# Kernel optimization log

Measured on AMD Instinct MI355X. Metric: run time of the kernel, lower is better.

## Reference

```python
import jax, jax.numpy as jnp
import numpy as np
from itertools import product as iter_product

N_QUBITS = 6
DIM = 2 ** N_QUBITS            # 64
N_GEN = DIM * DIM - 1          # 4095
DEPTH = 4
N_OBS = 15

_GENS = None

def _build_generators(n):
    I = np.eye(2, dtype=np.complex64)
    X = np.array([[0, 1], [1, 0]], np.complex64)
    Y = np.array([[0, -1j], [1j, 0]], np.complex64)
    Z = np.array([[1, 0], [0, -1]], np.complex64)
    P = [I, X, Y, Z]
    gens = []
    for idx in iter_product(range(4), repeat=n):
        if all(i == 0 for i in idx):
            continue
        m = P[idx[0]]
        for k in range(1, n):
            m = np.kron(m, P[idx[k]])
        gens.append(m)
    return jnp.asarray(np.stack(gens))  # [4^n-1, 2^n, 2^n] complex64

def _gens():
    global _GENS
    if _GENS is None:
        _GENS = _build_generators(N_QUBITS)
    return _GENS

def _apply_ry(psi, q, theta, n):
    # psi: [B, 2^n] complex; RY(theta) on qubit q
    B = psi.shape[0]
    x = psi.reshape(B, 2 ** q, 2, 2 ** (n - q - 1))
    c = jnp.cos(theta / 2)
    s = jnp.sin(theta / 2)
    s0, s1 = x[:, :, 0, :], x[:, :, 1, :]
    x = jnp.stack([c * s0 - s * s1, s * s0 + c * s1], axis=2)
    return x.reshape(B, -1)

def _apply_cnot(psi, c, t, n):
    # psi: [B, 2^n]; CNOT control c, target t
    B = psi.shape[0]
    x = psi.reshape((B,) + (2,) * n)
    ax_c, ax_t = 1 + c, 1 + t
    x0 = jnp.take(x, 0, axis=ax_c)
    x1 = jnp.take(x, 1, axis=ax_c)
    ax_t2 = ax_t - (1 if ax_t > ax_c else 0)
    x1 = jnp.flip(x1, axis=ax_t2)
    x = jnp.stack([x0, x1], axis=ax_c)
    return x.reshape(B, -1)

def _make_hermitians(A, B, D):
    # create_Hermitian vectorized over the m observables.
    # h[i,j] = A[idx]+iB[idx] for j<i (row-major lower-tri), h[i-1,i-1]=D[i];
    # then H = h + h^H.
    il, jl = jnp.tril_indices(DIM, -1)  # row-major order matches count+j loop
    di = jnp.arange(DIM - 1)

    def one(a, b, d):
        h = jnp.zeros((DIM, DIM), jnp.complex64)
        h = h.at[il, jl].set(a + 1j * b)
        h = h.at[di, di].set(d[1:].astype(jnp.complex64))
        return h + h.conj().T

    return jax.vmap(one)(A, B, D)  # [m, DIM, DIM]

def setup_inputs() -> dict:
    key = jax.random.key(0)
    ks = jax.random.split(key, 8)
    batch, input_dim, hidden = 256, 1024, 2047
    n_off = DIM * (DIM - 1) // 2  # 2016
    return {
        "x": jax.random.normal(ks[0], (batch, input_dim), jnp.float32),
        "W1": 0.02 * jax.random.normal(ks[1], (input_dim, hidden), jnp.float32),
        "b1": jnp.zeros((hidden,), jnp.float32),
        "W2": 0.02 * jax.random.normal(ks[2], (hidden, N_GEN), jnp.float32),
        "b2": jnp.zeros((N_GEN,), jnp.float32),
        "var_params": 0.01 * jax.random.normal(ks[3], (DEPTH, N_QUBITS), jnp.float32),
        "A": 2.0 * jax.random.normal(ks[4], (N_OBS, n_off), jnp.float32),
        "B": 2.0 * jax.random.normal(ks[5], (N_OBS, n_off), jnp.float32),
        "D": 2.0 * jax.random.normal(ks[6], (N_OBS, DIM), jnp.float32),
    }

def reference(x, W1, b1, W2, b2, var_params, A, B, D):
    n = N_QUBITS
    # encoding projection: Linear -> SiLU -> Linear
    h = jax.nn.silu(x @ W1 + b1)
    theta = h @ W2 + b2  # [batch, 4^n - 1]
    gens = _gens()  # [n_gen, dim, dim] complex64 (constant)
    # A_mat = sum_g theta_g G_g (Hermitian), U = exp(i A_mat)
    Amat = jnp.einsum('bg,gij->bij', theta.astype(jnp.complex64), gens)
    U = jax.vmap(jax.scipy.linalg.expm)(1j * Amat)  # [batch, dim, dim]
    psi = U[:, :, 0]  # apply to |0...0>
    # hardware-efficient VQC: RY layer + CNOT ring per depth
    for d in range(DEPTH):
        for q in range(n):
            psi = _apply_ry(psi, q, var_params[d, q], n)
        for q in range(n):
            psi = _apply_cnot(psi, q, (q + 1) % n, n)
    H = _make_hermitians(A, B, D)  # [m, dim, dim]
    # expectation <psi|H_w|psi>
    exp = jnp.einsum('bi,wij,bj->bw', psi.conj(), H, psi).real
    return exp  # [batch, n_observables]
```

## Files before the change

kernel.cpp:

```cpp
#include <hip/hip_runtime.h>
#include <math.h>

typedef unsigned short ushort_t;
typedef __attribute__((ext_vector_type(8))) short bf16x8_t;
typedef __attribute__((ext_vector_type(4))) float f32x4_t;

__device__ __forceinline__ void tsplit(float v, unsigned& h, unsigned& l) {
  unsigned u = __float_as_uint(v);
  h = u >> 16;
  float lo = v - __uint_as_float(u & 0xffff0000u);
  l = __float_as_uint(lo) >> 16;
}

__device__ __forceinline__ void split8(const float* p, bf16x8_t& hi, bf16x8_t& lo) {
#pragma unroll
  for (int e = 0; e < 8; ++e) {
    unsigned h, l;
    tsplit(p[e], h, l);
    hi[e] = (short)h;
    lo[e] = (short)l;
  }
}

#define LSTR 40

__global__ __launch_bounds__(512) void gemm1_kernel(
    const float* __restrict__ x, const float* __restrict__ W1,
    const float* __restrict__ b1,
    ushort_t* __restrict__ hh, ushort_t* __restrict__ hl) {
  __shared__ __align__(16) ushort_t As[2][32 * LSTR];
  __shared__ __align__(16) ushort_t Bs[2][64 * LSTR];
  const int t = threadIdx.x;
  const int lane = t & 63;
  const int wv = t >> 6;
  const int l15 = lane & 15;
  const int quad = lane >> 4;
  const int wm = wv & 1;
  const int wn = wv >> 1;
  const int m0 = (blockIdx.x >> 5) * 32;
  const int n0 = (blockIdx.x & 31) * 64;

  f32x4_t acc = (f32x4_t){0.f, 0.f, 0.f, 0.f};

  const int xrow = (t & 127) >> 2;
  const int xkq  = (t & 3) * 8;
  const int wu   = t - 128;
  const int wnx  = wu & 63;
  const int wkh  = (wu >> 6) & 3;
  const bool wok = (n0 + wnx) < 2047;

  for (int k0 = 0; k0 < 1024; k0 += 32) {
    if (t < 128) {
      const float* src = x + (size_t)(m0 + xrow) * 1024 + k0 + xkq;
      float p[8];
      float4 va = *(const float4*)src;
      float4 vb = *(const float4*)(src + 4);
      p[0] = va.x; p[1] = va.y; p[2] = va.z; p[3] = va.w;
      p[4] = vb.x; p[5] = vb.y; p[6] = vb.z; p[7] = vb.w;
      bf16x8_t hi, lo;
      split8(p, hi, lo);
      *(bf16x8_t*)&As[0][xrow * LSTR + xkq] = hi;
      *(bf16x8_t*)&As[1][xrow * LSTR + xkq] = lo;
    } else if (t < 384) {
      float p[8];
#pragma unroll
      for (int i = 0; i < 8; ++i) {
        int k = k0 + wkh * 8 + i;
        p[i] = wok ? W1[(size_t)k * 2047 + n0 + wnx] : 0.f;
      }
      bf16x8_t hi, lo;
      split8(p, hi, lo);
      *(bf16x8_t*)&Bs[0][wnx * LSTR + wkh * 8] = hi;
      *(bf16x8_t*)&Bs[1][wnx * LSTR + wkh * 8] = lo;
    }
    __syncthreads();
    const int nr = wn * 16 + l15;
    bf16x8_t bfh = *(const bf16x8_t*)&Bs[0][nr * LSTR + quad * 8];
    bf16x8_t bfl = *(const bf16x8_t*)&Bs[1][nr * LSTR + quad * 8];
    const int mr = wm * 16 + l15;
    bf16x8_t afh = *(const bf16x8_t*)&As[0][mr * LSTR + quad * 8];
    bf16x8_t afl = *(const bf16x8_t*)&As[1][mr * LSTR + quad * 8];
    acc = __builtin_amdgcn_mfma_f32_16x16x32_bf16(afh, bfh, acc, 0, 0, 0);
    acc = __builtin_amdgcn_mfma_f32_16x16x32_bf16(afh, bfl, acc, 0, 0, 0);
    acc = __builtin_amdgcn_mfma_f32_16x16x32_bf16(afl, bfh, acc, 0, 0, 0);
    __syncthreads();
  }
  const int col = n0 + wn * 16 + l15;
#pragma unroll
  for (int rg = 0; rg < 4; ++rg) {
    int row = m0 + wm * 16 + quad * 4 + rg;
    float v = acc[rg];
    if (col < 2047) {
      v += b1[col];
      v = v / (1.f + expf(-v));
    } else {
      v = 0.f;
    }
    unsigned h, l;
    tsplit(v, h, l);
    size_t o = (size_t)row * 2048 + col;
    hh[o] = (ushort_t)h;
    hl[o] = (ushort_t)l;
  }
}

__global__ __launch_bounds__(256) void gemm2k_kernel(
    const ushort_t* __restrict__ Ah, const ushort_t* __restrict__ Al,
    const float* __restrict__ W2,
    float* __restrict__ part) {
  __shared__ __align__(16) ushort_t Ab[2][64 * LSTR];
  __shared__ __align__(16) ushort_t Bb[2][64 * LSTR];
  const int t = threadIdx.x;
  const int lane = t & 63;
  const int wv = t >> 6;
  const int l15 = lane & 15;
  const int quad = lane >> 4;
  const int wm = wv >> 1, wn = wv & 1;
  const int m0 = blockIdx.y * 64;
  const int n0 = blockIdx.x * 64;
  const int ks = blockIdx.z;

  const int wu  = t - 128;
  const int bn  = wu & 63;
  const int bkh = (wu >> 6) & 1;
  const bool bok = (n0 + bn) < 4095;

  f32x4_t acc[2][2];
#pragma unroll
  for (int i = 0; i < 2; ++i)
#pragma unroll
    for (int j = 0; j < 2; ++j) acc[i][j] = (f32x4_t){0.f, 0.f, 0.f, 0.f};

  for (int kt = 0; kt < 16; ++kt) {
    const int k0 = ks * 512 + kt * 32;
    if (wv < 2) {
      const ushort_t* src = wv ? Al : Ah;
      ushort_t* dst = Ab[wv];
#pragma unroll
      for (int q = 0; q < 4; ++q) {
        int r = q * 16 + (lane >> 2);
        int c = (lane & 3) * 8;
        *(int4*)&dst[r * LSTR + c] =
            *(const int4*)(src + (size_t)(m0 + r) * 2048 + k0 + c);
      }
    } else {
      float p[16];
#pragma unroll
      for (int i = 0; i < 16; ++i) {
        int k = k0 + bkh * 16 + i;
        p[i] = (bok && k < 2047) ? W2[(size_t)k * 4095 + n0 + bn] : 0.f;
      }
#pragma unroll
      for (int half = 0; half < 2; ++half) {
        bf16x8_t hi, lo;
        split8(&p[half * 8], hi, lo);
        *(bf16x8_t*)&Bb[0][bn * LSTR + bkh * 16 + half * 8] = hi;
        *(bf16x8_t*)&Bb[1][bn * LSTR + bkh * 16 + half * 8] = lo;
      }
    }
    __syncthreads();
    bf16x8_t bfh[2], bfl[2];
#pragma unroll
    for (int j = 0; j < 2; ++j) {
      int nr = wn * 32 + j * 16 + l15;
      bfh[j] = *(const bf16x8_t*)&Bb[0][nr * LSTR + quad * 8];
      bfl[j] = *(const bf16x8_t*)&Bb[1][nr * LSTR + quad * 8];
    }
#pragma unroll
    for (int i = 0; i < 2; ++i) {
      int mr = wm * 32 + i * 16 + l15;
      bf16x8_t afh = *(const bf16x8_t*)&Ab[0][mr * LSTR + quad * 8];
      bf16x8_t afl = *(const bf16x8_t*)&Ab[1][mr * LSTR + quad * 8];
#pragma unroll
      for (int j = 0; j < 2; ++j) {
        acc[i][j] = __builtin_amdgcn_mfma_f32_16x16x32_bf16(
            afh, bfh[j], acc[i][j], 0, 0, 0);
        acc[i][j] = __builtin_amdgcn_mfma_f32_16x16x32_bf16(
            afh, bfl[j], acc[i][j], 0, 0, 0);
        acc[i][j] = __builtin_amdgcn_mfma_f32_16x16x32_bf16(
            afl, bfh[j], acc[i][j], 0, 0, 0);
      }
    }
    __syncthreads();
  }
  float* pbase = part + (size_t)ks * 256 * 4096;
#pragma unroll
  for (int i = 0; i < 2; ++i)
#pragma unroll
    for (int j = 0; j < 2; ++j) {
      int row0 = m0 + wm * 32 + i * 16 + quad * 4;
      int col = n0 + wn * 32 + j * 16 + l15;
#pragma unroll
      for (int rg = 0; rg < 4; ++rg)
        pbase[(size_t)(row0 + rg) * 4096 + col] = acc[i][j][rg];
    }
}

#define TM 64
#define TN 64
#define TK 16
__global__ __launch_bounds__(256) void gemm_tiled(
    const float* __restrict__ X, const float* __restrict__ W,
    const float* __restrict__ bias, float* __restrict__ out,
    int M, int N, int K, int ldx, int ldw, int ldo, int doSilu, int padN)
{
  __shared__ float Xs[TK][TM + 4];
  __shared__ float Ws[TK][TN + 4];
  const int t = threadIdx.x;
  const int n0 = blockIdx.x * TN;
  const int m0 = blockIdx.y * TM;
  const int tr = t >> 4, tc = t & 15;
  float acc[4][4];
#pragma unroll
  for (int i = 0; i < 4; ++i)
#pragma unroll
    for (int j = 0; j < 4; ++j) acc[i][j] = 0.f;
  const int xr = t >> 2, xk = (t & 3) * 4;
  const int wk = t >> 4, wc = (t & 15) * 4;
  for (int k0 = 0; k0 < K; k0 += TK) {
    {
      const float* xp = X + (size_t)(m0 + xr) * ldx + (k0 + xk);
      float xv[4];
      if (k0 + xk + 3 < K) {
        float4 v = *(const float4*)xp;
        xv[0] = v.x; xv[1] = v.y; xv[2] = v.z; xv[3] = v.w;
      } else {
#pragma unroll
        for (int e = 0; e < 4; ++e) xv[e] = (k0 + xk + e < K) ? xp[e] : 0.f;
      }
#pragma unroll
      for (int e = 0; e < 4; ++e) Xs[xk + e][xr] = xv[e];
    }
    {
      const int kk = k0 + wk;
      const float* wp = W + (size_t)kk * ldw + (n0 + wc);
      const bool kv = kk < K;
#pragma unroll
      for (int e = 0; e < 4; ++e) {
        int n = n0 + wc + e;
        Ws[wk][wc + e] = (kv && n < N) ? wp[e] : 0.f;
      }
    }
    __syncthreads();
#pragma unroll
    for (int k = 0; k < TK; ++k) {
      float4 av = *(const float4*)&Xs[k][tr * 4];
      float4 bv = *(const float4*)&Ws[k][tc * 4];
      float a4[4] = {av.x, av.y, av.z, av.w};
      float b4[4] = {bv.x, bv.y, bv.z, bv.w};
#pragma unroll
      for (int i = 0; i < 4; ++i)
#pragma unroll
        for (int j = 0; j < 4; ++j)
          acc[i][j] = fmaf(a4[i], b4[j], acc[i][j]);
    }
    __syncthreads();
  }
#pragma unroll
  for (int i = 0; i < 4; ++i) {
    const int mrow = m0 + tr * 4 + i;
    float* op = out + (size_t)mrow * ldo;
#pragma unroll
    for (int j = 0; j < 4; ++j) {
      const int n = n0 + tc * 4 + j;
      if (n < N) {
        float v = acc[i][j] + bias[n];
        if (doSilu) v = v / (1.f + expf(-v));
        op[n] = v;
      } else if (n < padN) {
        op[n] = 0.f;
      }
    }
  }
}

#define RS 72
#define PL (64 * RS)

__device__ __forceinline__ void qmm4(
    const ushort_t* __restrict__ Prm, const ushort_t* __restrict__ Qcm,
    float* ore, float* oim, int mt, int nt, int quad, int l15)
{
  f32x4_t aR = (f32x4_t){0.f, 0.f, 0.f, 0.f};
  f32x4_t aN = (f32x4_t){0.f, 0.f, 0.f, 0.f};
  f32x4_t aI = (f32x4_t){0.f, 0.f, 0.f, 0.f};
#pragma unroll
  for (int kb = 0; kb < 2; ++kb) {
    const int ko = kb * 32 + quad * 8;
    const int ra = (mt * 16 + l15) * RS + ko;
    bf16x8_t arh = *(const bf16x8_t*)&Prm[0 * PL + ra];
    bf16x8_t arl = *(const bf16x8_t*)&Prm[1 * PL + ra];
    bf16x8_t aih = *(const bf16x8_t*)&Prm[2 * PL + ra];
    bf16x8_t ail = *(const bf16x8_t*)&Prm[3 * PL + ra];
    const int rb = (nt * 16 + l15) * RS + ko;
    bf16x8_t brh = *(const bf16x8_t*)&Qcm[0 * PL + rb];
    bf16x8_t brl = *(const bf16x8_t*)&Qcm[1 * PL + rb];
    bf16x8_t bih = *(const bf16x8_t*)&Qcm[2 * PL + rb];
    bf16x8_t bil = *(const bf16x8_t*)&Qcm[3 * PL + rb];
    aR = __builtin_amdgcn_mfma_f32_16x16x32_bf16(arh, brh, aR, 0, 0, 0);
    aR = __builtin_amdgcn_mfma_f32_16x16x32_bf16(arh, brl, aR, 0, 0, 0);
    aR = __builtin_amdgcn_mfma_f32_16x16x32_bf16(arl, brh, aR, 0, 0, 0);
    aN = __builtin_amdgcn_mfma_f32_16x16x32_bf16(aih, bih, aN, 0, 0, 0);
    aN = __builtin_amdgcn_mfma_f32_16x16x32_bf16(aih, bil, aN, 0, 0, 0);
    aN = __builtin_amdgcn_mfma_f32_16x16x32_bf16(ail, bih, aN, 0, 0, 0);
    aI = __builtin_amdgcn_mfma_f32_16x16x32_bf16(arh, bih, aI, 0, 0, 0);
    aI = __builtin_amdgcn_mfma_f32_16x16x32_bf16(arh, bil, aI, 0, 0, 0);
    aI = __builtin_amdgcn_mfma_f32_16x16x32_bf16(arl, bih, aI, 0, 0, 0);
    aI = __builtin_amdgcn_mfma_f32_16x16x32_bf16(aih, brh, aI, 0, 0, 0);
    aI = __builtin_amdgcn_mfma_f32_16x16x32_bf16(aih, brl, aI, 0, 0, 0);
    aI = __builtin_amdgcn_mfma_f32_16x16x32_bf16(ail, brh, aI, 0, 0, 0);
  }
#pragma unroll
  for (int rg = 0; rg < 4; ++rg) {
    ore[rg] = aR[rg] - aN[rg];
    oim[rg] = aI[rg];
  }
}

__device__ __forceinline__ void stage_rm4(
    ushort_t* rm, const float* re, const float* im, int mt, int nt,
    int quad, int l15)
{
  unsigned rh[4], rl[4], ih[4], il[4];
#pragma unroll
  for (int rg = 0; rg < 4; ++rg) {
    tsplit(re[rg], rh[rg], rl[rg]);
    tsplit(im[rg], ih[rg], il[rg]);
  }
#pragma unroll
  for (int rg = 0; rg < 4; ++rg) {
    int idx = (mt * 16 + quad * 4 + rg) * RS + nt * 16 + l15;
    rm[0 * PL + idx] = (ushort_t)rh[rg];
    rm[1 * PL + idx] = (ushort_t)rl[rg];
    rm[2 * PL + idx] = (ushort_t)ih[rg];
    rm[3 * PL + idx] = (ushort_t)il[rg];
  }
}

__device__ __forceinline__ void stage_cm4(
    ushort_t* cm, const float* re, const float* im, int mt, int nt,
    int quad, int l15)
{
  unsigned rh[4], rl[4], ih[4], il[4];
#pragma unroll
  for (int rg = 0; rg < 4; ++rg) {
    tsplit(re[rg], rh[rg], rl[rg]);
    tsplit(im[rg], ih[rg], il[rg]);
  }
  int base = (nt * 16 + l15) * RS + mt * 16 + quad * 4;
  uint2 p;
  p.x = rh[0] | (rh[1] << 16); p.y = rh[2] | (rh[3] << 16);
  *(uint2*)&cm[0 * PL + base] = p;
  p.x = rl[0] | (rl[1] << 16); p.y = rl[2] | (rl[3] << 16);
  *(uint2*)&cm[1 * PL + base] = p;
  p.x = ih[0] | (ih[1] << 16); p.y = ih[2] | (ih[3] << 16);
  *(uint2*)&cm[2 * PL + base] = p;
  p.x = il[0] | (il[1] << 16); p.y = il[2] | (il[3] << 16);
  *(uint2*)&cm[3 * PL + base] = p;
}

__device__ __forceinline__ void stage_both4(
    ushort_t* rm, ushort_t* cm, const float* re, const float* im,
    int mt, int nt, int quad, int l15)
{
  stage_rm4(rm, re, im, mt, nt, quad, l15);
  stage_cm4(cm, re, im, mt, nt, quad, l15);
}

__global__ __launch_bounds__(1024, 4) void quantum_kernel(
    const float* __restrict__ pin,
    const float* __restrict__ b2g,
    const float* __restrict__ vp,
    const float* __restrict__ Aobs,
    const float* __restrict__ Bobs,
    const float* __restrict__ Dobs,
    float* __restrict__ out,
    int fused)
{
  __shared__ __align__(16) ushort_t PQ[2][8 * PL];
  __shared__ float ps[128];
  __shared__ float scr16[16];
  __shared__ float csb[24], snb[24];
  __shared__ float sAf;
  __shared__ int   sS;

  float*  thetas = (float*)&PQ[1][0];
  float2* Als    = (float2*)&PQ[0][0];

  const int t = threadIdx.x;
  const int b = blockIdx.x;
  const int lane = t & 63;
  const int w = t >> 6;
  const int quad = lane >> 4;
  const int l15 = lane & 15;
  const int mt = w >> 2, nt = w & 3;

  float ssq;
  {
    float4 v = ((const float4*)(pin + (size_t)b * 4096))[t];
    if (fused) {
#pragma unroll
      for (int k = 1; k < 4; ++k) {
        float4 u =
            ((const float4*)(pin + (size_t)k * 256 * 4096 + (size_t)b * 4096))[t];
        v.x += u.x; v.y += u.y; v.z += u.z; v.w += u.w;
      }
      int n0i = 4 * t;
      v.x += b2g[n0i];
      v.y += b2g[n0i + 1];
      v.z += b2g[n0i + 2];
      if (n0i + 3 < 4095) v.w += b2g[n0i + 3];
    }
    if (t == 1023) v.w = 0.f;
    thetas[4 * t + 0] = v.x; thetas[4 * t + 1] = v.y;
    thetas[4 * t + 2] = v.z; thetas[4 * t + 3] = v.w;
    ssq = v.x * v.x + v.y * v.y + v.z * v.z + v.w * v.w;
  }
#pragma unroll
  for (int mm = 1; mm < 64; mm <<= 1) ssq += __shfl_xor(ssq, mm);
  if (lane == 0) scr16[w] = ssq;
  __syncthreads();
  if (w == 0) {
    float s = (lane < 16) ? scr16[lane] : 0.f;
#pragma unroll
    for (int mm = 1; mm < 64; mm <<= 1) s += __shfl_xor(s, mm);
    if (lane == 0) {
      float frob = fmaxf(8.f * sqrtf(s), 1e-3f);
      sAf = frob;
      float bound = 0.30f * frob;
      int sc = (bound > 1.f) ? (int)ceilf(log2f(bound)) : 0;
      sS = sc < 0 ? 0 : (sc > 12 ? 12 : sc);
    }
  } else if (w == 1 && lane < 24) {
    float sn, cs;
    sincosf(vp[lane] * 0.5f, &sn, &cs);
    snb[lane] = sn;
    csb[lane] = cs;
  }
  __syncthreads();
  const int sPow = sS;

  for (int xx = 0; xx < 4; ++xx) {
    const int x = w + 16 * xx;
    const int z = lane;
    int g1 = 0;
#pragma unroll
    for (int bq = 0; bq < 6; ++bq) {
      int xb = (x >> bq) & 1, zb = (z >> bq) & 1;
      int dig = xb ? (zb ? 2 : 1) : (zb ? 3 : 0);
      g1 |= dig << (2 * bq);
    }
    float tv = (g1 == 0) ? 0.f : thetas[g1 - 1];
    int pc = __popc(x & z) & 3;
    float re, im;
    switch (pc) {
      case 0:  re = tv;  im = 0.f;  break;
      case 1:  re = 0.f; im = -tv;  break;
      case 2:  re = -tv; im = 0.f;  break;
      default: re = 0.f; im = tv;   break;
    }
#pragma unroll
    for (int mk = 1; mk < 64; mk <<= 1) {
      float ore = __shfl_xor(re, mk);
      float oim = __shfl_xor(im, mk);
      if (z & mk) { re = ore - re; im = oim - im; }
      else        { re = re + ore; im = im + oim; }
    }
    Als[z * 66 + (z ^ x)] = make_float2(re, im);
  }
  __syncthreads();

  const float scl = ldexpf(1.f, -sPow);
  float bre[4], bim[4];
#pragma unroll
  for (int rg = 0; rg < 4; ++rg) {
    int row = mt * 16 + quad * 4 + rg;
    int col = nt * 16 + l15;
    float2 v = Als[row * 66 + col];
    bre[rg] = -v.y * scl;
    bim[rg] =  v.x * scl;
  }
  __syncthreads();

  ushort_t* b0 = &PQ[0][0];
  ushort_t* b1 = &PQ[1][0];
  stage_both4(b0, b0 + 4 * PL, bre, bim, mt, nt, quad, l15);
  __syncthreads();
  float b2re[4], b2im[4];
  qmm4(b0, b0 + 4 * PL, b2re, b2im, mt, nt, quad, l15);
  stage_both4(b1, b1 + 4 * PL, b2re, b2im, mt, nt, quad, l15);
  __syncthreads();
  float b3re[4], b3im[4];
  qmm4(b1, b0 + 4 * PL, b3re, b3im, mt, nt, quad, l15);

  const float c3 = 1.f / 6.f, c4 = 1.f / 24.f, c5 = 1.f / 120.f;
  const float c6 = 1.f / 720.f, c7 = 1.f / 5040.f, c8 = 1.f / 40320.f;
  float s1re[4], s1im[4], p0re[4], p0im[4];
#pragma unroll
  for (int rg = 0; rg < 4; ++rg) {
    float dg = (mt == nt && l15 == quad * 4 + rg) ? 1.f : 0.f;
    s1re[rg] = c4 * dg + c5 * bre[rg] + c6 * b2re[rg] + c7 * b3re[rg];
    s1im[rg] =           c5 * bim[rg] + c6 * b2im[rg] + c7 * b3im[rg];
    p0re[rg] = dg + bre[rg] + 0.5f * b2re[rg] + c3 * b3re[rg];
    p0im[rg] =      bim[rg] + 0.5f * b2im[rg] + c3 * b3im[rg];
  }
  float b4re[4], b4im[4];
  qmm4(b1, b1 + 4 * PL, b4re, b4im, mt, nt, quad, l15);
#pragma unroll
  for (int rg = 0; rg < 4; ++rg) {
    s1re[rg] += c8 * b4re[rg];
    s1im[rg] += c8 * b4im[rg];
  }
  __syncthreads();
  stage_rm4(b0, s1re, s1im, mt, nt, quad, l15);
  stage_cm4(b0 + 4 * PL, b4re, b4im, mt, nt, quad, l15);
  __syncthreads();
  float ure[4], uim[4];
  qmm4(b0, b0 + 4 * PL, ure, uim, mt, nt, quad, l15);
#pragma unroll
  for (int rg = 0; rg < 4; ++rg) {
    ure[rg] += p0re[rg];
    uim[rg] += p0im[rg];
  }

  int cur = 1;
  for (int q = 0; q < sPow; ++q) {
    ushort_t* bb = &PQ[cur][0];
    stage_both4(bb, bb + 4 * PL, ure, uim, mt, nt, quad, l15);
    __syncthreads();
    qmm4(bb, bb + 4 * PL, ure, uim, mt, nt, quad, l15);
    cur ^= 1;
  }

  if (nt == 0 && l15 == 0) {
#pragma unroll
    for (int rg = 0; rg < 4; ++rg) {
      int row = mt * 16 + quad * 4 + rg;
      ps[2 * row] = ure[rg];
      ps[2 * row + 1] = uim[rg];
    }
  }
  __syncthreads();

  if (t < 64) {
    float pre = ps[2 * t], pim = ps[2 * t + 1];
#pragma unroll
    for (int d = 0; d < 4; ++d) {
#pragma unroll
      for (int q = 0; q < 6; ++q) {
        float s = snb[d * 6 + q], c = csb[d * 6 + q];
        int bpos = 5 - q;
        int bit = (t >> bpos) & 1;
        float ore = __shfl_xor(pre, 1 << bpos);
        float oim = __shfl_xor(pim, 1 << bpos);
        float sg = bit ? s : -s;
        pre = c * pre + sg * ore;
        pim = c * pim + sg * oim;
      }
#pragma unroll
      for (int q = 0; q < 6; ++q) {
        int bc = 5 - q;
        int bt = 5 - ((q + 1) % 6);
        float ore = __shfl_xor(pre, 1 << bt);
        float oim = __shfl_xor(pim, 1 << bt);
        int ctrl = (t >> bc) & 1;
        pre = ctrl ? ore : pre;
        pim = ctrl ? oim : pim;
      }
    }
    ps[2 * t] = pre; ps[2 * t + 1] = pim;
  }
  __syncthreads();

  float* Rt = (float*)&PQ[0][0];
  float* It = Rt + 2016;
  for (int p = t; p < 2016; p += 1024) {
    int i = (int)((1.f + sqrtf(8.f * (float)p + 1.f)) * 0.5f);
    while (i * (i - 1) / 2 > p) --i;
    while (i * (i + 1) / 2 <= p) ++i;
    int j = p - i * (i - 1) / 2;
    float pri = ps[2 * i], pii = ps[2 * i + 1];
    float prj = ps[2 * j], pij = ps[2 * j + 1];
    Rt[p] = pri * prj + pii * pij;
    It[p] = pri * pij - pii * prj;
  }
  __syncthreads();

  if (w < 15) {
    float xr = ps[2 * lane], xi = ps[2 * lane + 1];
    float mypsq = xr * xr + xi * xi;
    const float* Ap = Aobs + w * 2016;
    const float* Bp = Bobs + w * 2016;
    float part = 0.f;
    for (int p2 = lane; p2 < 1008; p2 += 64) {
      float2 a = *(const float2*)&Ap[2 * p2];
      float2 bb2 = *(const float2*)&Bp[2 * p2];
      float2 rt = *(const float2*)&Rt[2 * p2];
      float2 it = *(const float2*)&It[2 * p2];
      part += a.x * rt.x - bb2.x * it.x;
      part += a.y * rt.y - bb2.y * it.y;
    }
    if (lane < 63) part += Dobs[w * 64 + lane + 1] * mypsq;
#pragma unroll
    for (int mm = 1; mm < 64; mm <<= 1) part += __shfl_xor(part, mm);
    if (lane == 0) out[b * 15 + w] = 2.f * part;
  }
}

extern "C" void kernel_launch(void* const* d_in, const int* in_sizes, int n_in,
                              void* d_out, int out_size, void* d_ws, size_t ws_size,
                              hipStream_t stream) {
  const float* x  = (const float*)d_in[0];
  const float* W1 = (const float*)d_in[1];
  const float* b1 = (const float*)d_in[2];
  const float* W2 = (const float*)d_in[3];
  const float* b2 = (const float*)d_in[4];
  const float* vp = (const float*)d_in[5];
  const float* Ao = (const float*)d_in[6];
  const float* Bo = (const float*)d_in[7];
  const float* Do = (const float*)d_in[8];
  float* out = (float*)d_out;

  const size_t O_PT = 0;
  const size_t O_HH = 16777216;
  const size_t O_HL = 17825792;
  const size_t NEED = 18874368;

  if (ws_size >= NEED) {
    char* ws = (char*)d_ws;
    float* part16 = (float*)(ws + O_PT);
    ushort_t* hh  = (ushort_t*)(ws + O_HH);
    ushort_t* hl  = (ushort_t*)(ws + O_HL);

    gemm1_kernel<<<256, 512, 0, stream>>>(x, W1, b1, hh, hl);
    gemm2k_kernel<<<dim3(64, 4, 4), 256, 0, stream>>>(hh, hl, W2, part16);
    quantum_kernel<<<256, 1024, 0, stream>>>(part16, b2, vp, Ao, Bo, Do, out, 1);
  } else {
    float* h     = (float*)d_ws;
    float* theta = h + 256 * 2048;
    gemm_tiled<<<dim3(32, 4), 256, 0, stream>>>(
        x, W1, b1, h, 256, 2047, 1024, 1024, 2047, 2048, 1, 2048);
    gemm_tiled<<<dim3(64, 4), 256, 0, stream>>>(
        h, W2, b2, theta, 256, 4095, 2047, 2048, 4095, 4096, 0, 4096);
    quantum_kernel<<<256, 1024, 0, stream>>>(theta, b2, vp, Ao, Bo, Do, out, 0);
  }
}
```

Measured before the change: 174.2 us.

## Double-buffer shared tiles and prefetch next K-slice into registers in gemm2k

```diff
diff --git a/kernel.cpp b/kernel.cpp
--- a/kernel.cpp
+++ b/kernel.cpp
@@ -108,8 +108,8 @@
     const ushort_t* __restrict__ Ah, const ushort_t* __restrict__ Al,
     const float* __restrict__ W2,
     float* __restrict__ part) {
-  __shared__ __align__(16) ushort_t Ab[2][64 * LSTR];
-  __shared__ __align__(16) ushort_t Bb[2][64 * LSTR];
+  __shared__ __align__(16) ushort_t Ab[2][2][64 * LSTR];
+  __shared__ __align__(16) ushort_t Bb[2][2][64 * LSTR];
   const int t = threadIdx.x;
   const int lane = t & 63;
   const int wv = t >> 6;
@@ -124,6 +124,8 @@
   const int bn  = wu & 63;
   const int bkh = (wu >> 6) & 1;
   const bool bok = (n0 + bn) < 4095;
+  const int ar  = lane >> 2;
+  const int ac  = (lane & 3) * 8;
 
   f32x4_t acc[2][2];
 #pragma unroll
@@ -131,46 +133,69 @@
 #pragma unroll
     for (int j = 0; j < 2; ++j) acc[i][j] = (f32x4_t){0.f, 0.f, 0.f, 0.f};
 
-  for (int kt = 0; kt < 16; ++kt) {
-    const int k0 = ks * 512 + kt * 32;
+  int4  pa[4];
+  float pw[16];
+
+  {
+    const int k0 = ks * 512;
     if (wv < 2) {
       const ushort_t* src = wv ? Al : Ah;
-      ushort_t* dst = Ab[wv];
-#pragma unroll
-      for (int q = 0; q < 4; ++q) {
-        int r = q * 16 + (lane >> 2);
-        int c = (lane & 3) * 8;
-        *(int4*)&dst[r * LSTR + c] =
-            *(const int4*)(src + (size_t)(m0 + r) * 2048 + k0 + c);
-      }
+#pragma unroll
+      for (int q = 0; q < 4; ++q)
+        pa[q] = *(const int4*)(src + (size_t)(m0 + q * 16 + ar) * 2048 + k0 + ac);
     } else {
-      float p[16];
 #pragma unroll
       for (int i = 0; i < 16; ++i) {
         int k = k0 + bkh * 16 + i;
-        p[i] = (bok && k < 2047) ? W2[(size_t)k * 4095 + n0 + bn] : 0.f;
-      }
+        pw[i] = (bok && k < 2047) ? W2[(size_t)k * 4095 + n0 + bn] : 0.f;
+      }
+    }
+  }
+
+  int cur = 0;
+  for (int kt = 0; kt < 16; ++kt) {
+    if (wv < 2) {
+      ushort_t* dst = Ab[cur][wv];
+#pragma unroll
+      for (int q = 0; q < 4; ++q)
+        *(int4*)&dst[(q * 16 + ar) * LSTR + ac] = pa[q];
+    } else {
 #pragma unroll
       for (int half = 0; half < 2; ++half) {
         bf16x8_t hi, lo;
-        split8(&p[half * 8], hi, lo);
-        *(bf16x8_t*)&Bb[0][bn * LSTR + bkh * 16 + half * 8] = hi;
-        *(bf16x8_t*)&Bb[1][bn * LSTR + bkh * 16 + half * 8] = lo;
+        split8(&pw[half * 8], hi, lo);
+        *(bf16x8_t*)&Bb[cur][0][bn * LSTR + bkh * 16 + half * 8] = hi;
+        *(bf16x8_t*)&Bb[cur][1][bn * LSTR + bkh * 16 + half * 8] = lo;
       }
     }
     __syncthreads();
+    if (kt + 1 < 16) {
+      const int k0 = ks * 512 + (kt + 1) * 32;
+      if (wv < 2) {
+        const ushort_t* src = wv ? Al : Ah;
+#pragma unroll
+        for (int q = 0; q < 4; ++q)
+          pa[q] = *(const int4*)(src + (size_t)(m0 + q * 16 + ar) * 2048 + k0 + ac);
+      } else {
+#pragma unroll
+        for (int i = 0; i < 16; ++i) {
+          int k = k0 + bkh * 16 + i;
+          pw[i] = (bok && k < 2047) ? W2[(size_t)k * 4095 + n0 + bn] : 0.f;
+        }
+      }
+    }
     bf16x8_t bfh[2], bfl[2];
 #pragma unroll
     for (int j = 0; j < 2; ++j) {
       int nr = wn * 32 + j * 16 + l15;
-      bfh[j] = *(const bf16x8_t*)&Bb[0][nr * LSTR + quad * 8];
-      bfl[j] = *(const bf16x8_t*)&Bb[1][nr * LSTR + quad * 8];
+      bfh[j] = *(const bf16x8_t*)&Bb[cur][0][nr * LSTR + quad * 8];
+      bfl[j] = *(const bf16x8_t*)&Bb[cur][1][nr * LSTR + quad * 8];
     }
 #pragma unroll
     for (int i = 0; i < 2; ++i) {
       int mr = wm * 32 + i * 16 + l15;
-      bf16x8_t afh = *(const bf16x8_t*)&Ab[0][mr * LSTR + quad * 8];
-      bf16x8_t afl = *(const bf16x8_t*)&Ab[1][mr * LSTR + quad * 8];
+      bf16x8_t afh = *(const bf16x8_t*)&Ab[cur][0][mr * LSTR + quad * 8];
+      bf16x8_t afl = *(const bf16x8_t*)&Ab[cur][1][mr * LSTR + quad * 8];
 #pragma unroll
       for (int j = 0; j < 2; ++j) {
         acc[i][j] = __builtin_amdgcn_mfma_f32_16x16x32_bf16(
@@ -181,7 +206,7 @@
             afl, bfh[j], acc[i][j], 0, 0, 0);
       }
     }
-    __syncthreads();
+    cur ^= 1;
   }
   float* pbase = part + (size_t)ks * 256 * 4096;
 #pragma unroll
```

New measurement: 200.5 us. +15.1%, slower.
